# Performance work log

Measured on AMD Instinct MI355X. Metric: run time of the kernel, lower is better.

## Reference

```python
import jax, jax.numpy as jnp
import numpy as np

NUM_HEADS = 4


def setup_inputs() -> dict:
    key = jax.random.key(0)
    ks = jax.random.split(key, 5)
    B, C, L = 8, 128, 2048
    x = jax.random.normal(ks[0], (B, C, L), dtype=jnp.float32)
    # Conv1d(C, 3C, 1) == per-position linear; weight [3C, C], bias [3C]
    w_qkv = jax.random.normal(ks[1], (3 * C, C), dtype=jnp.float32) * (1.0 / np.sqrt(C))
    b_qkv = jax.random.normal(ks[2], (3 * C,), dtype=jnp.float32) * 0.01
    w_proj = jax.random.normal(ks[3], (C, C), dtype=jnp.float32) * (1.0 / np.sqrt(C))
    b_proj = jax.random.normal(ks[4], (C,), dtype=jnp.float32) * 0.01
    return {"x": x, "w_qkv": w_qkv, "b_qkv": b_qkv, "w_proj": w_proj, "b_proj": b_proj}


def reference(x, w_qkv, b_qkv, w_proj, b_proj):
    B, C, L = x.shape
    H = NUM_HEADS
    D = C // H
    scale = D ** -0.5
    # 1x1 conv qkv projection: [B, 3C, L]
    qkv = jnp.einsum('oc,bcl->bol', w_qkv, x) + b_qkv[None, :, None]
    # reshape (B,3,H,D,L) -> permute to (3,B,H,L,D)
    qkv = qkv.reshape(B, 3, H, D, L).transpose(1, 0, 2, 4, 3)
    q, k, v = qkv[0], qkv[1], qkv[2]  # each [B, H, L, D]
    attn = jax.nn.softmax(jnp.einsum('bhld,bhmd->bhlm', q, k) * scale, axis=-1)
    out = jnp.einsum('bhlm,bhmd->bhld', attn, v)  # [B, H, L, D]
    out = out.transpose(0, 1, 3, 2).reshape(B, C, L)
    out = jnp.einsum('oc,bcl->bol', w_proj, out) + b_proj[None, :, None]
    return out + x
```

## Files before the change

### kernel.cpp

```cpp
#include <hip/hip_runtime.h>

#define Bsz 8
#define Cdim 128
#define Lseq 2048
#define NH 4
#define HD 32
#define BH 32
#define QSCALE (0.17677669529663687f * 1.4426950408889634f)

typedef __bf16 bf16x8 __attribute__((ext_vector_type(8)));
typedef float f32x4 __attribute__((ext_vector_type(4)));
typedef unsigned u32x4 __attribute__((ext_vector_type(4)));

__device__ __forceinline__ float fexp2(float x) {
#if __has_builtin(__builtin_amdgcn_exp2f)
    return __builtin_amdgcn_exp2f(x);
#else
    return __expf(x * 0.6931471805599453f);
#endif
}

__device__ __forceinline__ unsigned short f2bf(float f) {
    unsigned u = __builtin_bit_cast(unsigned, f);
    u += 0x7FFFu + ((u >> 16) & 1u);
    return (unsigned short)(u >> 16);
}

__device__ __forceinline__ unsigned pack_bf16(float a, float b) {
    return (unsigned)f2bf(a) | ((unsigned)f2bf(b) << 16);
}

__device__ __forceinline__ unsigned pack_bf16_rtz(float a, float b) {
    return __builtin_amdgcn_perm(__builtin_bit_cast(unsigned, b),
                                 __builtin_bit_cast(unsigned, a), 0x07060302u);
}

__device__ __forceinline__ float bf_lo(unsigned u) {
    return __builtin_bit_cast(float, u << 16);
}
__device__ __forceinline__ float bf_hi(unsigned u) {
    return __builtin_bit_cast(float, u & 0xFFFF0000u);
}

#define MFMA16(A, B, C) __builtin_amdgcn_mfma_f32_16x16x32_bf16((A), (B), (C), 0, 0, 0)

__global__ __launch_bounds__(256) void qkv_kernel(const float* __restrict__ x,
        const float* __restrict__ w, const float* __restrict__ bias,
        unsigned short* __restrict__ qh, unsigned short* __restrict__ kh,
        unsigned short* __restrict__ vh) {
    __shared__ __attribute__((aligned(16))) unsigned short T[64][132];
    int bid = blockIdx.x;
    int og3 = bid % 3;
    int lt  = (bid / 3) & 31;
    int b   = bid / 96;
    int l0 = lt * 64;
    int t = threadIdx.x;
    int lane = t & 63, wv = t >> 6;
    int m16 = lane & 15, quad = lane >> 4;

    bf16x8 af[2][4];
    float bs[2][4];
    #pragma unroll
    for (int os = 0; os < 2; os++) {
        int orow = og3 * 128 + os * 64 + wv * 16;
        #pragma unroll
        for (int ks = 0; ks < 4; ks++) {
            const float* p = w + (size_t)(orow + m16) * Cdim + ks * 32 + quad * 8;
            float4 f0 = *(const float4*)p;
            float4 f1 = *(const float4*)(p + 4);
            u32x4 u = {pack_bf16(f0.x, f0.y), pack_bf16(f0.z, f0.w),
                       pack_bf16(f1.x, f1.y), pack_bf16(f1.z, f1.w)};
            af[os][ks] = __builtin_bit_cast(bf16x8, u);
        }
        #pragma unroll
        for (int r = 0; r < 4; r++) bs[os][r] = bias[orow + quad * 4 + r];
    }

    {
        int ll = t & 63, cg = t >> 6;
        const float* xb = x + (size_t)b * Cdim * Lseq + l0 + ll;
        #pragma unroll
        for (int i = 0; i < 16; i++) {
            int c = cg * 32 + 2 * i;
            float f0 = xb[(size_t)c * Lseq];
            float f1 = xb[(size_t)(c + 1) * Lseq];
            *(unsigned*)&T[ll][c] = pack_bf16(f0, f1);
        }
    }
    __syncthreads();

    #pragma unroll
    for (int ns = 0; ns < 4; ns++) {
        bf16x8 bx[4];
        #pragma unroll
        for (int ks = 0; ks < 4; ks++)
            bx[ks] = *(const bf16x8*)(&T[ns * 16 + m16][ks * 32 + quad * 8]);
        int l = l0 + ns * 16 + m16;
        #pragma unroll
        for (int os = 0; os < 2; os++) {
            f32x4 acc = {0.f, 0.f, 0.f, 0.f};
            #pragma unroll
            for (int ks = 0; ks < 4; ks++) acc = MFMA16(af[os][ks], bx[ks], acc);
            int oq = os * 64 + wv * 16 + quad * 4;
            if (og3 == 0) {
                int h = oq >> 5, d0 = oq & 31;
                uint2 u;
                u.x = pack_bf16((acc[0] + bs[os][0]) * QSCALE, (acc[1] + bs[os][1]) * QSCALE);
                u.y = pack_bf16((acc[2] + bs[os][2]) * QSCALE, (acc[3] + bs[os][3]) * QSCALE);
                *(uint2*)(qh + ((size_t)(b * NH + h) * Lseq + l) * HD + d0) = u;
            } else if (og3 == 1) {
                int h = oq >> 5, d0 = oq & 31;
                uint2 u;
                u.x = pack_bf16(acc[0] + bs[os][0], acc[1] + bs[os][1]);
                u.y = pack_bf16(acc[2] + bs[os][2], acc[3] + bs[os][3]);
                *(uint2*)(kh + ((size_t)(b * NH + h) * Lseq + l) * HD + d0) = u;
            } else {
                int kc = l >> 6, kk = l & 63;
                int half = kk >> 5, k32 = kk & 31;
                int q_, j_;
                if (k32 < 16) { q_ = k32 >> 2; j_ = k32 & 3; }
                else          { q_ = (k32 - 16) >> 2; j_ = 4 + ((k32 - 16) & 3); }
                int pos = half * 32 + q_ * 8 + j_;
                #pragma unroll
                for (int r = 0; r < 4; r++) {
                    int o = oq + r, h = o >> 5, d = o & 31;
                    vh[(((size_t)(b * NH + h) * 32 + kc) * HD + d) * 64 + pos] =
                        f2bf(acc[r] + bs[os][r]);
                }
            }
        }
    }
}

__global__ __launch_bounds__(256) void attn_kernel(
        const unsigned short* __restrict__ qh, const unsigned short* __restrict__ kh,
        const unsigned short* __restrict__ vh, unsigned short* __restrict__ po,
        float* __restrict__ pl) {
    __shared__ __attribute__((aligned(16))) char smem[19456];

    int bid = blockIdx.x;
    int xcd  = bid & 7;
    int rest = bid >> 3;
    int qt = rest & 31;
    int hb = rest >> 5;
    int bh = xcd + 8 * (hb & 3);
    int half = hb >> 2;

    int lane = threadIdx.x & 63;
    int wv   = threadIdx.x >> 6;
    int m16  = lane & 15;
    int quad = lane >> 4;
    int l0 = qt * 64;

    bf16x8 qf[4];
    #pragma unroll
    for (int qs = 0; qs < 4; qs++)
        qf[qs] = *(const bf16x8*)(qh + ((size_t)bh * Lseq + l0 + qs * 16 + m16) * HD + quad * 8);

    bf16x8 ones;
    #pragma unroll
    for (int i = 0; i < 8; i++) ones[i] = (__bf16)1.0f;

    f32x4 oacc[4][2];
    f32x4 lacc[4];
    #pragma unroll
    for (int qs = 0; qs < 4; qs++) {
        oacc[qs][0] = f32x4{0.f, 0.f, 0.f, 0.f};
        oacc[qs][1] = f32x4{0.f, 0.f, 0.f, 0.f};
        lacc[qs]    = f32x4{0.f, 0.f, 0.f, 0.f};
    }
    f32x4 zero = {0.f, 0.f, 0.f, 0.f};

    const unsigned short* kb = kh + (size_t)bh * Lseq * HD + m16 * HD + quad * 8;
    const unsigned short* vb = vh + (size_t)bh * 32 * HD * 64;
    int kbase = half * 1024 + wv * 256;

    auto load_kv = [&](int chunk, bf16x8* kf, bf16x8* vf) {
        int k0 = kbase + chunk * 64;
        #pragma unroll
        for (int t = 0; t < 4; t++)
            kf[t] = *(const bf16x8*)(kb + (size_t)(k0 + 16 * t) * HD);
        const unsigned short* vch = vb + (size_t)(k0 >> 6) * (HD * 64);
        vf[0] = *(const bf16x8*)(vch + m16 * 64 + quad * 8);
        vf[1] = *(const bf16x8*)(vch + (16 + m16) * 64 + quad * 8);
        vf[2] = *(const bf16x8*)(vch + m16 * 64 + 32 + quad * 8);
        vf[3] = *(const bf16x8*)(vch + (16 + m16) * 64 + 32 + quad * 8);
    };

    auto compute = [&](const bf16x8* kf, const bf16x8* vf) {
        #pragma unroll
        for (int qs = 0; qs < 4; qs++) {
            f32x4 s0 = MFMA16(kf[0], qf[qs], zero);
            f32x4 s1 = MFMA16(kf[1], qf[qs], zero);
            f32x4 s2 = MFMA16(kf[2], qf[qs], zero);
            f32x4 s3 = MFMA16(kf[3], qf[qs], zero);
            float p00 = fexp2(s0[0]), p01 = fexp2(s0[1]), p02 = fexp2(s0[2]), p03 = fexp2(s0[3]);
            float p10 = fexp2(s1[0]), p11 = fexp2(s1[1]), p12 = fexp2(s1[2]), p13 = fexp2(s1[3]);
            float p20 = fexp2(s2[0]), p21 = fexp2(s2[1]), p22 = fexp2(s2[2]), p23 = fexp2(s2[3]);
            float p30 = fexp2(s3[0]), p31 = fexp2(s3[1]), p32 = fexp2(s3[2]), p33 = fexp2(s3[3]);
            u32x4 lo = {pack_bf16_rtz(p00, p01), pack_bf16_rtz(p02, p03),
                        pack_bf16_rtz(p10, p11), pack_bf16_rtz(p12, p13)};
            u32x4 hi = {pack_bf16_rtz(p20, p21), pack_bf16_rtz(p22, p23),
                        pack_bf16_rtz(p30, p31), pack_bf16_rtz(p32, p33)};
            bf16x8 pfL = __builtin_bit_cast(bf16x8, lo);
            bf16x8 pfH = __builtin_bit_cast(bf16x8, hi);
            oacc[qs][0] = MFMA16(vf[0], pfL, oacc[qs][0]);
            oacc[qs][1] = MFMA16(vf[1], pfL, oacc[qs][1]);
            lacc[qs]    = MFMA16(ones,  pfL, lacc[qs]);
            oacc[qs][0] = MFMA16(vf[2], pfH, oacc[qs][0]);
            oacc[qs][1] = MFMA16(vf[3], pfH, oacc[qs][1]);
            lacc[qs]    = MFMA16(ones,  pfH, lacc[qs]);
        }
    };

    bf16x8 kA[4], vA[4], kB[4], vB[4];
    load_kv(0, kA, vA);
    load_kv(1, kB, vB);
    compute(kA, vA);
    load_kv(2, kA, vA);
    compute(kB, vB);
    load_kv(3, kB, vB);
    compute(kA, vA);
    compute(kB, vB);

    unsigned* red_o = (unsigned*)smem;
    float* red_l = (float*)(smem + 18432);
    #pragma unroll
    for (int qs = 0; qs < 4; qs++) {
        int row = qs * 16 + m16;
        unsigned* rw = red_o + (size_t)(wv * 64 + row) * 18;
        *(uint2*)(rw + 2 * quad) =
            make_uint2(pack_bf16_rtz(oacc[qs][0][0], oacc[qs][0][1]),
                       pack_bf16_rtz(oacc[qs][0][2], oacc[qs][0][3]));
        *(uint2*)(rw + 8 + 2 * quad) =
            make_uint2(pack_bf16_rtz(oacc[qs][1][0], oacc[qs][1][1]),
                       pack_bf16_rtz(oacc[qs][1][2], oacc[qs][1][3]));
        if (quad == 0) red_l[wv * 64 + row] = lacc[qs][0];
    }
    __syncthreads();

    int q = threadIdx.x >> 2;
    int s4 = (threadIdx.x & 3) * 4;
    float a8[8] = {0.f, 0.f, 0.f, 0.f, 0.f, 0.f, 0.f, 0.f};
    float lt = 0.f;
    #pragma unroll
    for (int w = 0; w < 4; w++) {
        const unsigned* rr = red_o + (size_t)(w * 64 + q) * 18 + s4;
        uint2 ua = *(const uint2*)(rr);
        uint2 ub = *(const uint2*)(rr + 2);
        a8[0] += bf_lo(ua.x); a8[1] += bf_hi(ua.x);
        a8[2] += bf_lo(ua.y); a8[3] += bf_hi(ua.y);
        a8[4] += bf_lo(ub.x); a8[5] += bf_hi(ub.x);
        a8[6] += bf_lo(ub.y); a8[7] += bf_hi(ub.y);
        lt += red_l[w * 64 + q];
    }
    int d0 = (threadIdx.x & 3) * 8;
    uint4 u;
    u.x = pack_bf16(a8[0], a8[1]);
    u.y = pack_bf16(a8[2], a8[3]);
    u.z = pack_bf16(a8[4], a8[5]);
    u.w = pack_bf16(a8[6], a8[7]);
    *(uint4*)(po + ((size_t)(half * BH + bh) * Lseq + l0 + q) * HD + d0) = u;
    if ((threadIdx.x & 3) == 0)
        pl[(size_t)(half * BH + bh) * Lseq + l0 + q] = lt;
}

__global__ __launch_bounds__(256) void proj_kernel(const float* __restrict__ wp,
        const unsigned short* __restrict__ po, const float* __restrict__ pl,
        const float* __restrict__ bias, const float* __restrict__ x,
        float* __restrict__ out) {
    __shared__ __attribute__((aligned(16))) unsigned short T[32][132];
    int bid = blockIdx.x;
    int ot = bid & 1;
    int nt = bid >> 1;
    int n0 = nt * 32;
    int t = threadIdx.x;

    {
        int nl = t >> 3, g = t & 7;
        int h = g >> 1, d0 = (g & 1) * 16;
        int n = n0 + nl, b = n >> 11, l = n & (Lseq - 1);
        int bh = b * NH + h;
        const unsigned short* p0 = po + ((size_t)bh * Lseq + l) * HD + d0;
        const unsigned short* p1 = po + ((size_t)(BH + bh) * Lseq + l) * HD + d0;
        float inv = 1.0f / (pl[(size_t)bh * Lseq + l] + pl[(size_t)(BH + bh) * Lseq + l]);
        uint4 a0 = *(const uint4*)p0, a1 = *(const uint4*)(p0 + 8);
        uint4 b0 = *(const uint4*)p1, b1 = *(const uint4*)(p1 + 8);
        uint4 u0, u1;
        u0.x = pack_bf16((bf_lo(a0.x) + bf_lo(b0.x)) * inv, (bf_hi(a0.x) + bf_hi(b0.x)) * inv);
        u0.y = pack_bf16((bf_lo(a0.y) + bf_lo(b0.y)) * inv, (bf_hi(a0.y) + bf_hi(b0.y)) * inv);
        u0.z = pack_bf16((bf_lo(a0.z) + bf_lo(b0.z)) * inv, (bf_hi(a0.z) + bf_hi(b0.z)) * inv);
        u0.w = pack_bf16((bf_lo(a0.w) + bf_lo(b0.w)) * inv, (bf_hi(a0.w) + bf_hi(b0.w)) * inv);
        u1.x = pack_bf16((bf_lo(a1.x) + bf_lo(b1.x)) * inv, (bf_hi(a1.x) + bf_hi(b1.x)) * inv);
        u1.y = pack_bf16((bf_lo(a1.y) + bf_lo(b1.y)) * inv, (bf_hi(a1.y) + bf_hi(b1.y)) * inv);
        u1.z = pack_bf16((bf_lo(a1.z) + bf_lo(b1.z)) * inv, (bf_hi(a1.z) + bf_hi(b1.z)) * inv);
        u1.w = pack_bf16((bf_lo(a1.w) + bf_lo(b1.w)) * inv, (bf_hi(a1.w) + bf_hi(b1.w)) * inv);
        int c0 = g * 16;
        *(uint4*)&T[nl][c0]     = u0;
        *(uint4*)&T[nl][c0 + 8] = u1;
    }

    int lane = t & 63;
    int wv = t >> 6;
    int m16 = lane & 15, quad = lane >> 4;
    int o0 = ot * 64 + wv * 16;

    bf16x8 af[4];
    #pragma unroll
    for (int ks = 0; ks < 4; ks++) {
        const float* p = wp + (size_t)(o0 + m16) * Cdim + ks * 32 + quad * 8;
        float4 f0 = *(const float4*)p;
        float4 f1 = *(const float4*)(p + 4);
        u32x4 u = {pack_bf16(f0.x, f0.y), pack_bf16(f0.z, f0.w),
                   pack_bf16(f1.x, f1.y), pack_bf16(f1.z, f1.w)};
        af[ks] = __builtin_bit_cast(bf16x8, u);
    }
    float bs[4];
    #pragma unroll
    for (int r = 0; r < 4; r++) bs[r] = bias[o0 + quad * 4 + r];
    int oq = o0 + quad * 4;

    __syncthreads();

    #pragma unroll
    for (int lt2 = 0; lt2 < 2; lt2++) {
        int n = n0 + lt2 * 16 + m16;
        bf16x8 bx[4];
        #pragma unroll
        for (int ks = 0; ks < 4; ks++)
            bx[ks] = *(const bf16x8*)(&T[lt2 * 16 + m16][ks * 32 + quad * 8]);
        f32x4 acc = {0.f, 0.f, 0.f, 0.f};
        #pragma unroll
        for (int ks = 0; ks < 4; ks++) acc = MFMA16(af[ks], bx[ks], acc);
        int b = n >> 11, l = n & (Lseq - 1);
        #pragma unroll
        for (int r = 0; r < 4; r++) {
            size_t xi = ((size_t)b * Cdim + oq + r) * Lseq + l;
            out[xi] = acc[r] + bs[r] + x[xi];
        }
    }
}

extern "C" void kernel_launch(void* const* d_in, const int* in_sizes, int n_in,
                              void* d_out, int out_size, void* d_ws, size_t ws_size,
                              hipStream_t stream) {
    const float* x      = (const float*)d_in[0];
    const float* w_qkv  = (const float*)d_in[1];
    const float* b_qkv  = (const float*)d_in[2];
    const float* w_proj = (const float*)d_in[3];
    const float* b_proj = (const float*)d_in[4];
    float* out = (float*)d_out;

    const size_t E = (size_t)BH * Lseq * HD;
    unsigned short* qh = (unsigned short*)d_ws;
    unsigned short* kh = qh + E;
    unsigned short* vh = kh + E;
    unsigned short* po = vh + E;
    float* pl = (float*)(po + 2 * E);

    qkv_kernel<<<dim3(768), dim3(256), 0, stream>>>(x, w_qkv, b_qkv, qh, kh, vh);
    attn_kernel<<<dim3(2048), dim3(256), 0, stream>>>(qh, kh, vh, po, pl);
    proj_kernel<<<dim3(1024), dim3(256), 0, stream>>>(w_proj, po, pl, b_proj, x, out);
}
```

Measured before the change: 117.2 us.

## Drop key-split in attention, normalize in-kernel, compute row sums on VALU

Removes the two-way split over the key dimension, so each block covers all 2048 keys (each wave handles 512) and the grid is halved. Normalization moves into the attention kernel, which lets the projection kernel read the final bf16 output straight from global memory, without the LDS merge of partial results and without a barrier. The softmax denominator now comes from VALU adds of the exp values rather than extra MFMAs against a ones vector. In exchange, per-block work doubles and occupancy may drop with only 1024 blocks. The denominator is summed from fp32 values while the numerator uses bf16-truncated weights, a slight numeric mismatch.

```diff
diff --git a/kernel.cpp b/kernel.cpp
--- a/kernel.cpp
+++ b/kernel.cpp
@@ -134,17 +134,15 @@
 
 __global__ __launch_bounds__(256) void attn_kernel(
         const unsigned short* __restrict__ qh, const unsigned short* __restrict__ kh,
-        const unsigned short* __restrict__ vh, unsigned short* __restrict__ po,
-        float* __restrict__ pl) {
-    __shared__ __attribute__((aligned(16))) char smem[19456];
+        const unsigned short* __restrict__ vh, unsigned short* __restrict__ oo) {
+    __shared__ __attribute__((aligned(16))) char smem[22528];
 
     int bid = blockIdx.x;
     int xcd  = bid & 7;
     int rest = bid >> 3;
     int qt = rest & 31;
-    int hb = rest >> 5;
-    int bh = xcd + 8 * (hb & 3);
-    int half = hb >> 2;
+    int g  = rest >> 5;
+    int bh = xcd + 8 * g;
 
     int lane = threadIdx.x & 63;
     int wv   = threadIdx.x >> 6;
@@ -157,23 +155,19 @@
     for (int qs = 0; qs < 4; qs++)
         qf[qs] = *(const bf16x8*)(qh + ((size_t)bh * Lseq + l0 + qs * 16 + m16) * HD + quad * 8);
 
-    bf16x8 ones;
-    #pragma unroll
-    for (int i = 0; i < 8; i++) ones[i] = (__bf16)1.0f;
-
     f32x4 oacc[4][2];
-    f32x4 lacc[4];
+    float sacc[4];
     #pragma unroll
     for (int qs = 0; qs < 4; qs++) {
         oacc[qs][0] = f32x4{0.f, 0.f, 0.f, 0.f};
         oacc[qs][1] = f32x4{0.f, 0.f, 0.f, 0.f};
-        lacc[qs]    = f32x4{0.f, 0.f, 0.f, 0.f};
+        sacc[qs]    = 0.f;
     }
     f32x4 zero = {0.f, 0.f, 0.f, 0.f};
 
     const unsigned short* kb = kh + (size_t)bh * Lseq * HD + m16 * HD + quad * 8;
     const unsigned short* vb = vh + (size_t)bh * 32 * HD * 64;
-    int kbase = half * 1024 + wv * 256;
+    int kbase = wv * 512;
 
     auto load_kv = [&](int chunk, bf16x8* kf, bf16x8* vf) {
         int k0 = kbase + chunk * 64;
@@ -198,6 +192,11 @@
             float p10 = fexp2(s1[0]), p11 = fexp2(s1[1]), p12 = fexp2(s1[2]), p13 = fexp2(s1[3]);
             float p20 = fexp2(s2[0]), p21 = fexp2(s2[1]), p22 = fexp2(s2[2]), p23 = fexp2(s2[3]);
             float p30 = fexp2(s3[0]), p31 = fexp2(s3[1]), p32 = fexp2(s3[2]), p33 = fexp2(s3[3]);
+            float r0 = (p00 + p01) + (p02 + p03);
+            float r1 = (p10 + p11) + (p12 + p13);
+            float r2 = (p20 + p21) + (p22 + p23);
+            float r3 = (p30 + p31) + (p32 + p33);
+            sacc[qs] += (r0 + r1) + (r2 + r3);
             u32x4 lo = {pack_bf16_rtz(p00, p01), pack_bf16_rtz(p02, p03),
                         pack_bf16_rtz(p10, p11), pack_bf16_rtz(p12, p13)};
             u32x4 hi = {pack_bf16_rtz(p20, p21), pack_bf16_rtz(p22, p23),
@@ -206,20 +205,20 @@
             bf16x8 pfH = __builtin_bit_cast(bf16x8, hi);
             oacc[qs][0] = MFMA16(vf[0], pfL, oacc[qs][0]);
             oacc[qs][1] = MFMA16(vf[1], pfL, oacc[qs][1]);
-            lacc[qs]    = MFMA16(ones,  pfL, lacc[qs]);
             oacc[qs][0] = MFMA16(vf[2], pfH, oacc[qs][0]);
             oacc[qs][1] = MFMA16(vf[3], pfH, oacc[qs][1]);
-            lacc[qs]    = MFMA16(ones,  pfH, lacc[qs]);
         }
     };
 
     bf16x8 kA[4], vA[4], kB[4], vB[4];
     load_kv(0, kA, vA);
     load_kv(1, kB, vB);
-    compute(kA, vA);
-    load_kv(2, kA, vA);
-    compute(kB, vB);
-    load_kv(3, kB, vB);
+    compute(kA, vA); load_kv(2, kA, vA);
+    compute(kB, vB); load_kv(3, kB, vB);
+    compute(kA, vA); load_kv(4, kA, vA);
+    compute(kB, vB); load_kv(5, kB, vB);
+    compute(kA, vA); load_kv(6, kA, vA);
+    compute(kB, vB); load_kv(7, kB, vB);
     compute(kA, vA);
     compute(kB, vB);
 
@@ -235,7 +234,7 @@
         *(uint2*)(rw + 8 + 2 * quad) =
             make_uint2(pack_bf16_rtz(oacc[qs][1][0], oacc[qs][1][1]),
                        pack_bf16_rtz(oacc[qs][1][2], oacc[qs][1][3]));
-        if (quad == 0) red_l[wv * 64 + row] = lacc[qs][0];
+        red_l[(wv * 64 + row) * 4 + quad] = sacc[qs];
     }
     __syncthreads();
 
@@ -252,54 +251,27 @@
         a8[2] += bf_lo(ua.y); a8[3] += bf_hi(ua.y);
         a8[4] += bf_lo(ub.x); a8[5] += bf_hi(ub.x);
         a8[6] += bf_lo(ub.y); a8[7] += bf_hi(ub.y);
-        lt += red_l[w * 64 + q];
-    }
+        float4 lv = *(const float4*)(red_l + (size_t)(w * 64 + q) * 4);
+        lt += (lv.x + lv.y) + (lv.z + lv.w);
+    }
+    float inv = 1.0f / lt;
     int d0 = (threadIdx.x & 3) * 8;
     uint4 u;
-    u.x = pack_bf16(a8[0], a8[1]);
-    u.y = pack_bf16(a8[2], a8[3]);
-    u.z = pack_bf16(a8[4], a8[5]);
-    u.w = pack_bf16(a8[6], a8[7]);
-    *(uint4*)(po + ((size_t)(half * BH + bh) * Lseq + l0 + q) * HD + d0) = u;
-    if ((threadIdx.x & 3) == 0)
-        pl[(size_t)(half * BH + bh) * Lseq + l0 + q] = lt;
+    u.x = pack_bf16(a8[0] * inv, a8[1] * inv);
+    u.y = pack_bf16(a8[2] * inv, a8[3] * inv);
+    u.z = pack_bf16(a8[4] * inv, a8[5] * inv);
+    u.w = pack_bf16(a8[6] * inv, a8[7] * inv);
+    *(uint4*)(oo + ((size_t)bh * Lseq + l0 + q) * HD + d0) = u;
 }
 
 __global__ __launch_bounds__(256) void proj_kernel(const float* __restrict__ wp,
-        const unsigned short* __restrict__ po, const float* __restrict__ pl,
-        const float* __restrict__ bias, const float* __restrict__ x,
-        float* __restrict__ out) {
-    __shared__ __attribute__((aligned(16))) unsigned short T[32][132];
+        const unsigned short* __restrict__ oo, const float* __restrict__ bias,
+        const float* __restrict__ x, float* __restrict__ out) {
     int bid = blockIdx.x;
     int ot = bid & 1;
     int nt = bid >> 1;
     int n0 = nt * 32;
     int t = threadIdx.x;
-
-    {
-        int nl = t >> 3, g = t & 7;
-        int h = g >> 1, d0 = (g & 1) * 16;
-        int n = n0 + nl, b = n >> 11, l = n & (Lseq - 1);
-        int bh = b * NH + h;
-        const unsigned short* p0 = po + ((size_t)bh * Lseq + l) * HD + d0;
-        const unsigned short* p1 = po + ((size_t)(BH + bh) * Lseq + l) * HD + d0;
-        float inv = 1.0f / (pl[(size_t)bh * Lseq + l] + pl[(size_t)(BH + bh) * Lseq + l]);
-        uint4 a0 = *(const uint4*)p0, a1 = *(const uint4*)(p0 + 8);
-        uint4 b0 = *(const uint4*)p1, b1 = *(const uint4*)(p1 + 8);
-        uint4 u0, u1;
-        u0.x = pack_bf16((bf_lo(a0.x) + bf_lo(b0.x)) * inv, (bf_hi(a0.x) + bf_hi(b0.x)) * inv);
-        u0.y = pack_bf16((bf_lo(a0.y) + bf_lo(b0.y)) * inv, (bf_hi(a0.y) + bf_hi(b0.y)) * inv);
-        u0.z = pack_bf16((bf_lo(a0.z) + bf_lo(b0.z)) * inv, (bf_hi(a0.z) + bf_hi(b0.z)) * inv);
-        u0.w = pack_bf16((bf_lo(a0.w) + bf_lo(b0.w)) * inv, (bf_hi(a0.w) + bf_hi(b0.w)) * inv);
-        u1.x = pack_bf16((bf_lo(a1.x) + bf_lo(b1.x)) * inv, (bf_hi(a1.x) + bf_hi(b1.x)) * inv);
-        u1.y = pack_bf16((bf_lo(a1.y) + bf_lo(b1.y)) * inv, (bf_hi(a1.y) + bf_hi(b1.y)) * inv);
-        u1.z = pack_bf16((bf_lo(a1.z) + bf_lo(b1.z)) * inv, (bf_hi(a1.z) + bf_hi(b1.z)) * inv);
-        u1.w = pack_bf16((bf_lo(a1.w) + bf_lo(b1.w)) * inv, (bf_hi(a1.w) + bf_hi(b1.w)) * inv);
-        int c0 = g * 16;
-        *(uint4*)&T[nl][c0]     = u0;
-        *(uint4*)&T[nl][c0 + 8] = u1;
-    }
-
     int lane = t & 63;
     int wv = t >> 6;
     int m16 = lane & 15, quad = lane >> 4;
@@ -320,19 +292,17 @@
     for (int r = 0; r < 4; r++) bs[r] = bias[o0 + quad * 4 + r];
     int oq = o0 + quad * 4;
 
-    __syncthreads();
-
     #pragma unroll
     for (int lt2 = 0; lt2 < 2; lt2++) {
         int n = n0 + lt2 * 16 + m16;
+        int b = n >> 11, l = n & (Lseq - 1);
         bf16x8 bx[4];
         #pragma unroll
         for (int ks = 0; ks < 4; ks++)
-            bx[ks] = *(const bf16x8*)(&T[lt2 * 16 + m16][ks * 32 + quad * 8]);
+            bx[ks] = *(const bf16x8*)(oo + ((size_t)(b * NH + ks) * Lseq + l) * HD + quad * 8);
         f32x4 acc = {0.f, 0.f, 0.f, 0.f};
         #pragma unroll
         for (int ks = 0; ks < 4; ks++) acc = MFMA16(af[ks], bx[ks], acc);
-        int b = n >> 11, l = n & (Lseq - 1);
         #pragma unroll
         for (int r = 0; r < 4; r++) {
             size_t xi = ((size_t)b * Cdim + oq + r) * Lseq + l;
@@ -355,10 +325,9 @@
     unsigned short* qh = (unsigned short*)d_ws;
     unsigned short* kh = qh + E;
     unsigned short* vh = kh + E;
-    unsigned short* po = vh + E;
-    float* pl = (float*)(po + 2 * E);
+    unsigned short* oo = vh + E;
 
     qkv_kernel<<<dim3(768), dim3(256), 0, stream>>>(x, w_qkv, b_qkv, qh, kh, vh);
-    attn_kernel<<<dim3(2048), dim3(256), 0, stream>>>(qh, kh, vh, po, pl);
-    proj_kernel<<<dim3(1024), dim3(256), 0, stream>>>(w_proj, po, pl, b_proj, x, out);
-}
+    attn_kernel<<<dim3(1024), dim3(256), 0, stream>>>(qh, kh, vh, oo);
+    proj_kernel<<<dim3(1024), dim3(256), 0, stream>>>(w_proj, oo, b_proj, x, out);
+}
```

Result: no change. 114.9 us (-1.9%).
